# Kernel tuning notes

Measured on AMD Instinct MI355X. Metric: run time of the kernel, lower is better.

The kernel has to match this reference:

```python
import jax, jax.numpy as jnp
import numpy as np

KERNEL = 5
PAD = (KERNEL - 1) // 2  # fixed_padding with dilation=1: pad_beg = pad_end = 2


def setup_inputs() -> dict:
    key = jax.random.key(0)
    kx, kw = jax.random.split(key)
    x = jax.random.normal(kx, (4, 4, 1024, 1024), dtype=jnp.float32)
    weight = jax.random.normal(kw, (4, 4, KERNEL, KERNEL), dtype=jnp.float32)
    return {"x": x, "weight": weight}


def reference(x, weight):
    """Morphological dilation2d: out[b,o,h,w] = max_{c,i,j} (x_pad[b,c,h+i,w+j] + w[o,c,i,j]).

    Equivalent to the torch unfold + broadcast-add + max over dim C*k*k, but computed
    as a fused sliding-window max-plus without materializing the im2col tensor.
    """
    B, C, H, W = x.shape
    k = weight.shape[-1]
    xp = jnp.pad(x, ((0, 0), (0, 0), (PAD, PAD), (PAD, PAD)))  # zero pad, same as F.pad
    out = None
    for i in range(k):
        for j in range(k):
            patch = xp[:, :, i:i + H, j:j + W]          # (B, C, H, W)
            w_ij = weight[:, :, i, j]                    # (O, C)
            # max over in_channels of (x + w) for this tap
            val = jnp.max(patch[:, None] + w_ij[None, :, :, None, None], axis=2)  # (B, O, H, W)
            out = val if out is None else jnp.maximum(out, val)
    return out
```

## Files before the change

### kernel.cpp

```cpp
#include <hip/hip_runtime.h>


constexpr int Himg = 1024, Wimg = 1024, Cin = 4, Cout = 4, Kn = 5;
constexpr int TH = 8, TW = 128;
constexpr int LR = TH + 4;
constexpr int LC = TW + 8;
constexpr int LC4 = LC / 4;
constexpr int NW = Cout * Cin * Kn * Kn;

typedef float v2f __attribute__((ext_vector_type(2)));

__device__ __align__(16) v2f wdup[Cin * Kn * Cout * Kn];

__global__ void reorg_w(const float* __restrict__ w) {
  int idx = threadIdx.x;
  if (idx < NW) {
    int o  = idx / (Cin * Kn * Kn);
    int r  = idx % (Cin * Kn * Kn);
    int c  = r / (Kn * Kn);
    int r2 = r % (Kn * Kn);
    int i  = r2 / Kn, j = r2 % Kn;
    float v = w[idx];
    v2f p; p.x = v; p.y = v;
    wdup[((c * Kn + i) * Cout + o) * Kn + j] = p;
  }
}

__device__ __forceinline__ float max5(float a, float b, float c, float d, float e) {
  return fmaxf(fmaxf(a, b), fmaxf(c, fmaxf(d, e)));
}

__global__ __launch_bounds__(256) void morph(const float* __restrict__ x,
                                             float* __restrict__ out) {
  __shared__ __align__(16) float xs[Cin][LR][LC];
  const int tid = threadIdx.x;
  const int tile_w0 = blockIdx.x * TW;
  const int tile_r0 = blockIdx.y * TH;
  const int b = blockIdx.z;

  for (int idx = tid; idx < Cin * LR * LC4; idx += 256) {
    const int c   = idx / (LR * LC4);
    const int rem = idx - c * (LR * LC4);
    const int row = rem / LC4;
    const int ch  = rem - row * LC4;
    const int gr  = tile_r0 - 2 + row;
    const int gc  = tile_w0 - 4 + ch * 4;
    float4 v = make_float4(0.f, 0.f, 0.f, 0.f);
    if ((unsigned)gr < (unsigned)Himg) {
      const float* src = x + ((size_t)(b * Cin + c) * Himg + gr) * Wimg;
      if (gc >= 0 && gc <= Wimg - 4) {
        v = *(const float4*)(src + gc);
      } else {
        if ((unsigned)(gc + 0) < (unsigned)Wimg) v.x = src[gc + 0];
        if ((unsigned)(gc + 1) < (unsigned)Wimg) v.y = src[gc + 1];
        if ((unsigned)(gc + 2) < (unsigned)Wimg) v.z = src[gc + 2];
        if ((unsigned)(gc + 3) < (unsigned)Wimg) v.w = src[gc + 3];
      }
    }
    *(float4*)&xs[c][row][ch * 4] = v;
  }
  __syncthreads();

  const int tx = tid & 31;
  const int ty = tid >> 5;

  float acc[Cout][4];
#pragma unroll
  for (int o = 0; o < Cout; ++o)
#pragma unroll
    for (int p = 0; p < 4; ++p) acc[o][p] = -3.4e38f;

#define ACC_O(O)                                                                          \
  do {                                                                                    \
    v2f p01[5], p23[5];                                                                   \
    _Pragma("unroll") for (int j = 0; j < 5; ++j) {                                       \
      v2f wb = wdp[(O) * Kn + j];                                                         \
      p01[j] = a2[j] + wb;                                                                \
      p23[j] = b2[j] + wb;                                                                \
    }                                                                                     \
    acc[O][0] = fmaxf(acc[O][0], max5(p01[0].x, p01[1].x, p01[2].x, p01[3].x, p01[4].x)); \
    acc[O][1] = fmaxf(acc[O][1], max5(p01[0].y, p01[1].y, p01[2].y, p01[3].y, p01[4].y)); \
    acc[O][2] = fmaxf(acc[O][2], max5(p23[0].x, p23[1].x, p23[2].x, p23[3].x, p23[4].x)); \
    acc[O][3] = fmaxf(acc[O][3], max5(p23[0].y, p23[1].y, p23[2].y, p23[3].y, p23[4].y)); \
  } while (0)

#pragma unroll 1
  for (int c = 0; c < Cin; ++c) {
#pragma unroll
    for (int i = 0; i < Kn; ++i) {
      const float* rowp = &xs[c][ty + i][tx * 4];
      float4 q0 = *(const float4*)(rowp);
      float4 q1 = *(const float4*)(rowp + 4);
      float4 q2 = *(const float4*)(rowp + 8);
      float win[12] = {q0.x, q0.y, q0.z, q0.w, q1.x, q1.y, q1.z, q1.w,
                       q2.x, q2.y, q2.z, q2.w};

      v2f a2[5], b2[5];
#pragma unroll
      for (int j = 0; j < 5; ++j) {
        a2[j].x = win[2 + j]; a2[j].y = win[3 + j];
        b2[j].x = win[4 + j]; b2[j].y = win[5 + j];
      }

      const v2f* wdp = wdup + (c * Kn + i) * Cout * Kn;

      ACC_O(0);
      ACC_O(1);
      ACC_O(2);
      ACC_O(3);
    }
  }
#undef ACC_O

  const int r = tile_r0 + ty;
  const int gc0 = tile_w0 + tx * 4;
#pragma unroll
  for (int o = 0; o < Cout; ++o) {
    float4 res = make_float4(acc[o][0], acc[o][1], acc[o][2], acc[o][3]);
    *(float4*)&out[((size_t)(b * Cout + o) * Himg + r) * Wimg + gc0] = res;
  }
}

extern "C" void kernel_launch(void* const* d_in, const int* in_sizes, int n_in,
                              void* d_out, int out_size, void* d_ws, size_t ws_size,
                              hipStream_t stream) {
  const float* x = (const float*)d_in[0];
  const float* w = (const float*)d_in[1];
  float* out = (float*)d_out;

  reorg_w<<<dim3(1), dim3(512), 0, stream>>>(w);

  dim3 grid(Wimg / TW, Himg / TH, 4);
  morph<<<grid, dim3(256), 0, stream>>>(x, out);
}
```

Measured before the change: 155.8 us.

## Compute four output rows per thread and stage one input channel at a time

Each thread now computes 4 output rows (tile height grows from 8 to 32), so every shared-memory row read serves up to 4 output rows instead of 1. The halo overhead per output row drops from (8+4)/8 to (32+4)/32, cutting redundant global loads. Shared memory holds one channel at a time with a sync per channel, which keeps LDS use small but serializes load and compute. Register pressure rises (64 accumulators per thread) and launch bounds ask for 4 blocks per CU, and the grid has 4x fewer blocks.

```diff
diff --git a/kernel.cpp b/kernel.cpp
--- a/kernel.cpp
+++ b/kernel.cpp
@@ -2,8 +2,9 @@
 
 
 constexpr int Himg = 1024, Wimg = 1024, Cin = 4, Cout = 4, Kn = 5;
-constexpr int TH = 8, TW = 128;
-constexpr int LR = TH + 4;
+constexpr int TH = 32, TW = 128;
+constexpr int RPT = 4;
+constexpr int LRows = TH + 4;
 constexpr int LC = TW + 8;
 constexpr int LC4 = LC / 4;
 constexpr int NW = Cout * Cin * Kn * Kn;
@@ -30,65 +31,67 @@
   return fmaxf(fmaxf(a, b), fmaxf(c, fmaxf(d, e)));
 }
 
-__global__ __launch_bounds__(256) void morph(const float* __restrict__ x,
-                                             float* __restrict__ out) {
-  __shared__ __align__(16) float xs[Cin][LR][LC];
+__global__ __launch_bounds__(256, 4) void morph(const float* __restrict__ x,
+                                                float* __restrict__ out) {
+  __shared__ __align__(16) float xs[LRows][LC];
   const int tid = threadIdx.x;
   const int tile_w0 = blockIdx.x * TW;
   const int tile_r0 = blockIdx.y * TH;
   const int b = blockIdx.z;
 
-  for (int idx = tid; idx < Cin * LR * LC4; idx += 256) {
-    const int c   = idx / (LR * LC4);
-    const int rem = idx - c * (LR * LC4);
-    const int row = rem / LC4;
-    const int ch  = rem - row * LC4;
-    const int gr  = tile_r0 - 2 + row;
-    const int gc  = tile_w0 - 4 + ch * 4;
-    float4 v = make_float4(0.f, 0.f, 0.f, 0.f);
-    if ((unsigned)gr < (unsigned)Himg) {
-      const float* src = x + ((size_t)(b * Cin + c) * Himg + gr) * Wimg;
-      if (gc >= 0 && gc <= Wimg - 4) {
-        v = *(const float4*)(src + gc);
-      } else {
-        if ((unsigned)(gc + 0) < (unsigned)Wimg) v.x = src[gc + 0];
-        if ((unsigned)(gc + 1) < (unsigned)Wimg) v.y = src[gc + 1];
-        if ((unsigned)(gc + 2) < (unsigned)Wimg) v.z = src[gc + 2];
-        if ((unsigned)(gc + 3) < (unsigned)Wimg) v.w = src[gc + 3];
-      }
-    }
-    *(float4*)&xs[c][row][ch * 4] = v;
-  }
-  __syncthreads();
-
   const int tx = tid & 31;
   const int ty = tid >> 5;
 
-  float acc[Cout][4];
+  float acc[Cout][RPT][4];
 #pragma unroll
   for (int o = 0; o < Cout; ++o)
 #pragma unroll
-    for (int p = 0; p < 4; ++p) acc[o][p] = -3.4e38f;
+    for (int k = 0; k < RPT; ++k)
+#pragma unroll
+      for (int p = 0; p < 4; ++p) acc[o][k][p] = -3.4e38f;
 
-#define ACC_O(O)                                                                          \
+#define ACC_KO(K, O, WDP)                                                                 \
   do {                                                                                    \
     v2f p01[5], p23[5];                                                                   \
     _Pragma("unroll") for (int j = 0; j < 5; ++j) {                                       \
-      v2f wb = wdp[(O) * Kn + j];                                                         \
+      v2f wb = (WDP)[(O) * Kn + j];                                                       \
       p01[j] = a2[j] + wb;                                                                \
       p23[j] = b2[j] + wb;                                                                \
     }                                                                                     \
-    acc[O][0] = fmaxf(acc[O][0], max5(p01[0].x, p01[1].x, p01[2].x, p01[3].x, p01[4].x)); \
-    acc[O][1] = fmaxf(acc[O][1], max5(p01[0].y, p01[1].y, p01[2].y, p01[3].y, p01[4].y)); \
-    acc[O][2] = fmaxf(acc[O][2], max5(p23[0].x, p23[1].x, p23[2].x, p23[3].x, p23[4].x)); \
-    acc[O][3] = fmaxf(acc[O][3], max5(p23[0].y, p23[1].y, p23[2].y, p23[3].y, p23[4].y)); \
+    acc[O][K][0] = fmaxf(acc[O][K][0], max5(p01[0].x, p01[1].x, p01[2].x, p01[3].x, p01[4].x)); \
+    acc[O][K][1] = fmaxf(acc[O][K][1], max5(p01[0].y, p01[1].y, p01[2].y, p01[3].y, p01[4].y)); \
+    acc[O][K][2] = fmaxf(acc[O][K][2], max5(p23[0].x, p23[1].x, p23[2].x, p23[3].x, p23[4].x)); \
+    acc[O][K][3] = fmaxf(acc[O][K][3], max5(p23[0].y, p23[1].y, p23[2].y, p23[3].y, p23[4].y)); \
   } while (0)
 
 #pragma unroll 1
   for (int c = 0; c < Cin; ++c) {
+    __syncthreads();
+
+    for (int idx = tid; idx < LRows * LC4; idx += 256) {
+      const int row = idx / LC4;
+      const int ch  = idx - row * LC4;
+      const int gr  = tile_r0 - 2 + row;
+      const int gc  = tile_w0 - 4 + ch * 4;
+      float4 v = make_float4(0.f, 0.f, 0.f, 0.f);
+      if ((unsigned)gr < (unsigned)Himg) {
+        const float* src = x + ((size_t)(b * Cin + c) * Himg + gr) * Wimg;
+        if (gc >= 0 && gc <= Wimg - 4) {
+          v = *(const float4*)(src + gc);
+        } else {
+          if ((unsigned)(gc + 0) < (unsigned)Wimg) v.x = src[gc + 0];
+          if ((unsigned)(gc + 1) < (unsigned)Wimg) v.y = src[gc + 1];
+          if ((unsigned)(gc + 2) < (unsigned)Wimg) v.z = src[gc + 2];
+          if ((unsigned)(gc + 3) < (unsigned)Wimg) v.w = src[gc + 3];
+        }
+      }
+      *(float4*)&xs[row][ch * 4] = v;
+    }
+    __syncthreads();
+
 #pragma unroll
-    for (int i = 0; i < Kn; ++i) {
-      const float* rowp = &xs[c][ty + i][tx * 4];
+    for (int dr = 0; dr < RPT + 4; ++dr) {
+      const float* rowp = &xs[ty * RPT + dr][tx * 4];
       float4 q0 = *(const float4*)(rowp);
       float4 q1 = *(const float4*)(rowp + 4);
       float4 q2 = *(const float4*)(rowp + 8);
@@ -102,23 +105,30 @@
         b2[j].x = win[4 + j]; b2[j].y = win[5 + j];
       }
 
-      const v2f* wdp = wdup + (c * Kn + i) * Cout * Kn;
-
-      ACC_O(0);
-      ACC_O(1);
-      ACC_O(2);
-      ACC_O(3);
+#pragma unroll
+      for (int k = 0; k < RPT; ++k) {
+        const int i = dr - k;
+        if (i >= 0 && i < Kn) {
+          const v2f* wdp = wdup + (c * Kn + i) * Cout * Kn;
+          ACC_KO(k, 0, wdp);
+          ACC_KO(k, 1, wdp);
+          ACC_KO(k, 2, wdp);
+          ACC_KO(k, 3, wdp);
+        }
+      }
     }
   }
-#undef ACC_O
+#undef ACC_KO
 
-  const int r = tile_r0 + ty;
   const int gc0 = tile_w0 + tx * 4;
 #pragma unroll
-  for (int o = 0; o < Cout; ++o) {
-    float4 res = make_float4(acc[o][0], acc[o][1], acc[o][2], acc[o][3]);
-    *(float4*)&out[((size_t)(b * Cout + o) * Himg + r) * Wimg + gc0] = res;
-  }
+  for (int o = 0; o < Cout; ++o)
+#pragma unroll
+    for (int k = 0; k < RPT; ++k) {
+      const int r = tile_r0 + ty * RPT + k;
+      float4 res = make_float4(acc[o][k][0], acc[o][k][1], acc[o][k][2], acc[o][k][3]);
+      *(float4*)&out[((size_t)(b * Cout + o) * Himg + r) * Wimg + gc0] = res;
+    }
 }
 
 extern "C" void kernel_launch(void* const* d_in, const int* in_sizes, int n_in,
```

Measured after the change: 189.3 us. +21.5%, slower.
